# Performance work log

Measured on AMD Instinct MI355X. Metric: run time of the kernel, lower is better.

Reference implementation:

```python
import jax, jax.numpy as jnp
import numpy as np

B, T, E = 2, 2048, 2048
H, KV, D = 16, 4, 128
N_REP = H // KV
WINDOW = 512
BASE_THETA = 10000.0
MIN_VAL = -1e9


def _rope_cos_sin(seq_len, dim, dtype):
    inv_freq = 1.0 / (BASE_THETA ** (jnp.arange(0, dim, 2, dtype=jnp.float32) / dim))
    ang = jnp.arange(seq_len, dtype=jnp.float32)[:, None] * inv_freq[None, :]  # [T, D/2]
    return jnp.cos(ang).astype(dtype), jnp.sin(ang).astype(dtype)


def _apply_rope(x, cos, sin):
    # x: [B, T, h, D]; rotate-half convention
    x1, x2 = jnp.split(x, 2, axis=-1)
    c = cos[None, :, None, :]
    s = sin[None, :, None, :]
    return jnp.concatenate([x1 * c - x2 * s, x2 * c + x1 * s], axis=-1)


def setup_inputs() -> dict:
    key = jax.random.key(0)
    k1, k2, k3, k4, k5 = jax.random.split(key, 5)
    std = 0.02 / np.sqrt(2 * 24)
    return {
        "x": jax.random.normal(k1, (B, T, E), dtype=jnp.float32),
        "Wq": jax.random.normal(k2, (H * D, E), dtype=jnp.float32) * std,
        "Wk": jax.random.normal(k3, (KV * D, E), dtype=jnp.float32) * std,
        "Wv": jax.random.normal(k4, (KV * D, E), dtype=jnp.float32) * std,
        "Wo": jax.random.normal(k5, (E, E), dtype=jnp.float32) * std,
    }


def reference(x, Wq, Wk, Wv, Wo):
    b, t, e = x.shape
    scale = 1.0 / jnp.sqrt(jnp.float32(D))

    q = (x @ Wq.T).reshape(b, t, H, D)
    k = (x @ Wk.T).reshape(b, t, KV, D)
    v = (x @ Wv.T).reshape(b, t, KV, D)

    cos, sin = _rope_cos_sin(t, D, x.dtype)
    q = _apply_rope(q, cos, sin)
    k = _apply_rope(k, cos, sin)

    # GQA: repeat kv heads to match query heads
    k = jnp.repeat(k, N_REP, axis=2)  # [B, T, H, D]
    v = jnp.repeat(v, N_REP, axis=2)

    scores = jnp.einsum("bqhd,bkhd->bhqk", q, k) * scale  # [B, H, T, T]

    # sliding-window causal additive mask (offset=0)
    rows = jnp.arange(t)[:, None]
    cols = jnp.arange(t)[None, :]
    valid = (cols <= rows) & ((rows - cols) < WINDOW)
    mask = jnp.where(valid, 0.0, MIN_VAL).astype(x.dtype)  # [T, T]
    scores = scores + mask[None, None, :, :]

    attn = jax.nn.softmax(scores, axis=-1)
    out = jnp.einsum("bhqk,bkhd->bqhd", attn, v).reshape(b, t, H * D)
    return out @ Wo.T
```

## Files before the change

kernel.cpp:

```cpp
#include <hip/hip_runtime.h>
#include <hip/hip_bf16.h>
#include <cstdint>

#define TSEQ 2048
#define NB   2
#define NH   16
#define NKV  4
#define HD   128
#define EMB  2048
#define WIN  512

typedef unsigned short u16;
typedef __attribute__((ext_vector_type(8))) short s16x8;
typedef __attribute__((ext_vector_type(4))) float f32x4;
typedef __attribute__((ext_vector_type(16))) float f32x16;
typedef __attribute__((ext_vector_type(4))) unsigned short u16x4;
typedef __attribute__((ext_vector_type(8))) unsigned short u16x8;

__device__ __forceinline__ u16 f2bf(float x) {
    unsigned u = __builtin_bit_cast(unsigned, x);
    u += 0x7fffu + ((u >> 16) & 1u);
    return (u16)(u >> 16);
}
__device__ __forceinline__ float bf2f(u16 u) {
    return __builtin_bit_cast(float, ((unsigned)u) << 16);
}
__device__ __forceinline__ float ex2(float x) {
    return __builtin_amdgcn_exp2f(x);
}

__device__ __forceinline__ void gld_lds16(const void* g, void* l) {
    __builtin_amdgcn_global_load_lds(
        (__attribute__((address_space(1))) void*)(void*)(g),
        (__attribute__((address_space(3))) void*)(l),
        16, 0, 0);
}

__device__ __forceinline__ f32x4 mfma16(s16x8 a, s16x8 b, f32x4 c) {
    return __builtin_amdgcn_mfma_f32_16x16x32_bf16(a, b, c, 0, 0, 0);
}
__device__ __forceinline__ f32x16 mfma32(s16x8 a, s16x8 b, f32x16 c) {
    return __builtin_amdgcn_mfma_f32_32x32x16_bf16(a, b, c, 0, 0, 0);
}

template <int CTRL>
__device__ __forceinline__ float dpp_movf(float x) {
    return __builtin_bit_cast(float,
        __builtin_amdgcn_update_dpp(0, __builtin_bit_cast(int, x), CTRL, 0xF, 0xF, true));
}
__device__ __forceinline__ float dpp_max16(float x) {
    x = fmaxf(x, dpp_movf<0xB1>(x));
    x = fmaxf(x, dpp_movf<0x4E>(x));
    x = fmaxf(x, dpp_movf<0x128>(x));
    x = fmaxf(x, dpp_movf<0x124>(x));
    return x;
}
__device__ __forceinline__ float dpp_sum16(float x) {
    x += dpp_movf<0xB1>(x);
    x += dpp_movf<0x4E>(x);
    x += dpp_movf<0x128>(x);
    x += dpp_movf<0x124>(x);
    return x;
}

__global__ void cast_all(const float* __restrict__ x,  const float* __restrict__ wq,
                         const float* __restrict__ wk, const float* __restrict__ wv,
                         const float* __restrict__ wo,
                         u16* __restrict__ xb, u16* __restrict__ wqb,
                         u16* __restrict__ wkvb, u16* __restrict__ wob,
                         float* __restrict__ tab) {
    if (blockIdx.x >= 18432) {
        int i = (blockIdx.x - 18432) * 256 + threadIdx.x;
        int t = i >> 6, d = i & 63;
        float inv = __expf(-(float)d * (9.210340371976184f / 64.0f));
        float s, c;
        sincosf((float)t * inv, &s, &c);
        tab[i] = c;
        tab[131072 + i] = s;
        return;
    }
    long i = ((long)blockIdx.x * 256 + threadIdx.x) * 4;
    const float* s; u16* d; long off;
    if (i < 8388608L)        { s = x;  d = xb;             off = i; }
    else if (i < 12582912L)  { s = wq; d = wqb;            off = i - 8388608L; }
    else if (i < 13631488L)  { s = wk; d = wkvb;           off = i - 12582912L; }
    else if (i < 14680064L)  { s = wv; d = wkvb + 1048576; off = i - 13631488L; }
    else                     { s = wo; d = wob;            off = i - 14680064L; }
    float4 v = *(const float4*)(s + off);
    u16x4 o;
    o[0] = f2bf(v.x); o[1] = f2bf(v.y); o[2] = f2bf(v.z); o[3] = f2bf(v.w);
    *(u16x4*)(d + off) = o;
}

template <int MODE>
__global__ __launch_bounds__(256) void gemm_bt(const u16* __restrict__ A, const u16* __restrict__ B,
                                               void* __restrict__ Cp, u16* __restrict__ vtp,
                                               u16* __restrict__ kp,
                                               int M, int N, int K) {
    __shared__ __align__(16) u16 smem[16384];
    u16* As = smem;
    u16* Bs = smem + 8192;
    const int tid  = threadIdx.x;
    const int lane = tid & 63;
    const int w    = tid >> 6;
    const int l31  = lane & 31;
    const int half = lane >> 5;
    const int wr   = w >> 1, wc = w & 1;

    const int srow   = w * 8 + (lane >> 3);
    const int schunk = lane & 7;
    const u16* agp[4];
    const u16* bgp[4];
#pragma unroll
    for (int s = 0; s < 4; s++) {
        const int row = s * 32 + srow;
        const int sig = ((row >> 1) ^ (row >> 2)) & 7;
        agp[s] = A + (size_t)(blockIdx.y * 128 + row) * K + (schunk ^ sig) * 8;
        bgp[s] = B + (size_t)(blockIdx.x * 128 + row) * K + (schunk ^ sig) * 8;
    }

    int sigA[2], sigB[2];
#pragma unroll
    for (int i = 0; i < 2; i++) {
        const int ra = wr * 64 + i * 32 + l31;
        sigA[i] = ((ra >> 1) ^ (ra >> 2)) & 7;
        const int rb = wc * 64 + i * 32 + l31;
        sigB[i] = ((rb >> 1) ^ (rb >> 2)) & 7;
    }

    f32x16 acc[2][2];
#pragma unroll
    for (int i = 0; i < 2; i++)
#pragma unroll
        for (int j = 0; j < 2; j++)
#pragma unroll
            for (int r = 0; r < 16; r++)
                acc[i][j][r] = 0.f;

    for (int k0 = 0; k0 < K; k0 += 64) {
#pragma unroll
        for (int s = 0; s < 4; s++) {
            gld_lds16(agp[s], (char*)As + (s * 32 + w * 8) * 128);
            agp[s] += 64;
        }
#pragma unroll
        for (int s = 0; s < 4; s++) {
            gld_lds16(bgp[s], (char*)Bs + (s * 32 + w * 8) * 128);
            bgp[s] += 64;
        }
        __syncthreads();
        s16x8 af[2][4], bf[2][4];
#pragma unroll
        for (int i = 0; i < 2; i++)
#pragma unroll
            for (int ks = 0; ks < 4; ks++)
                af[i][ks] = *(const s16x8*)((char*)As + (wr * 64 + i * 32 + l31) * 128 +
                                            ((half + ks * 2) ^ sigA[i]) * 16);
#pragma unroll
        for (int j = 0; j < 2; j++)
#pragma unroll
            for (int ks = 0; ks < 4; ks++)
                bf[j][ks] = *(const s16x8*)((char*)Bs + (wc * 64 + j * 32 + l31) * 128 +
                                            ((half + ks * 2) ^ sigB[j]) * 16);
#pragma unroll
        for (int ks = 0; ks < 4; ks++)
#pragma unroll
            for (int i = 0; i < 2; i++)
#pragma unroll
                for (int j = 0; j < 2; j++)
                    acc[i][j] = mfma32(af[i][ks], bf[j][ks], acc[i][j]);
        __syncthreads();
    }

    const int row0 = blockIdx.y * 128 + wr * 64;
    const int col0 = blockIdx.x * 128 + wc * 64 + l31;

    if (MODE == 0) {
#pragma unroll
        for (int i = 0; i < 2; i++)
#pragma unroll
            for (int j = 0; j < 2; j++)
#pragma unroll
                for (int r = 0; r < 16; r++) {
                    const int crow = row0 + i * 32 + (r & 3) + 8 * (r >> 2) + 4 * half;
                    ((float*)Cp)[(size_t)crow * N + col0 + j * 32] = acc[i][j][r];
                }
    } else {
        if (blockIdx.x < 16) {
#pragma unroll
            for (int i = 0; i < 2; i++)
#pragma unroll
                for (int j = 0; j < 2; j++)
#pragma unroll
                    for (int r = 0; r < 16; r++) {
                        const int crow = row0 + i * 32 + (r & 3) + 8 * (r >> 2) + 4 * half;
                        ((u16*)Cp)[(size_t)crow * 2048 + col0 + j * 32] = f2bf(acc[i][j][r]);
                    }
        } else if (blockIdx.x < 20) {
            const int kcol0 = col0 - 2048;
#pragma unroll
            for (int i = 0; i < 2; i++)
#pragma unroll
                for (int j = 0; j < 2; j++)
#pragma unroll
                    for (int r = 0; r < 16; r++) {
                        const int crow = row0 + i * 32 + (r & 3) + 8 * (r >> 2) + 4 * half;
                        kp[(size_t)crow * 512 + kcol0 + j * 32] = f2bf(acc[i][j][r]);
                    }
        } else {
            const int kvi = blockIdx.x - 20;
            const int bb  = (blockIdx.y * 128) >> 11;
            const int tl0 = (blockIdx.y * 128) & (TSEQ - 1);
            u16* tr = smem;
#pragma unroll
            for (int p = 0; p < 2; p++) {
                __syncthreads();
                if (wc == p) {
#pragma unroll
                    for (int i = 0; i < 2; i++)
#pragma unroll
                        for (int j = 0; j < 2; j++)
#pragma unroll
                            for (int r = 0; r < 16; r++) {
                                const int tl = wr * 64 + i * 32 + (r & 3) + 8 * (r >> 2) + 4 * half;
                                tr[(j * 32 + l31) * 136 + tl] = f2bf(acc[i][j][r]);
                            }
                }
                __syncthreads();
#pragma unroll
                for (int s = 0; s < 4; s++) {
                    int slot = s * 256 + tid;
                    int dr = slot >> 4;
                    int tc = slot & 15;
                    u16x8 val = *(const u16x8*)(tr + dr * 136 + tc * 8);
                    *(u16x8*)(vtp + ((size_t)((bb * NKV + kvi) * HD + p * 64 + dr)) * TSEQ +
                              tl0 + tc * 8) = val;
                }
            }
        }
    }
}

__global__ void rope_k(u16* __restrict__ buf, const float* __restrict__ tab) {
    int i = blockIdx.x * 256 + threadIdx.x;
    int d   = i & 63;
    int hh  = (i >> 6) & 3;
    int row = i >> 8;
    int t   = row & (TSEQ - 1);
    size_t base = (size_t)row * 512 + hh * HD + d;
    float x1 = bf2f(buf[base]);
    float x2 = bf2f(buf[base + 64]);
    float c = tab[t * 64 + d];
    float s = tab[131072 + t * 64 + d];
    buf[base]      = f2bf(x1 * c - x2 * s);
    buf[base + 64] = f2bf(x2 * c + x1 * s);
}

__global__ __launch_bounds__(256, 4) void attn_kernel(const u16* __restrict__ qb, const u16* __restrict__ kb,
                                                      const u16* __restrict__ vt, const float* __restrict__ tab,
                                                      u16* __restrict__ ao) {
    __shared__ __align__(16) char smem[40960];
    u16* ks = (u16*)smem;
    u16* vs = (u16*)(smem + 16384);
    u16* Pl = (u16*)(smem + 32768);

    const int tid  = threadIdx.x;
    const int w    = tid >> 6;
    const int lane = tid & 63;
    const int l15  = lane & 15;
    const int quad = lane >> 4;
    const int id   = blockIdx.x;
    const int kv   = id & 3;
    const int b    = (id >> 2) & 1;
    const int q0   = (id >> 3) * 16;
    const int h    = kv * 4 + w;
    u16* Pw = Pl + w * 1024;
    const float scale2 = 0.1275174089593282f;

    const u16* kbase = kb + (size_t)b * TSEQ * 512 + kv * HD;
    const u16* vbase = vt + (size_t)(b * NKV + kv) * HD * TSEQ;

    s16x8 aq[4];
    {
        const u16* qrow = qb + (size_t)(b * TSEQ + q0 + l15) * EMB + h * HD + quad * 8;
        const float* ct = tab + (size_t)(q0 + l15) * 64 + quad * 8;
        float qf[4][8], cs[2][8], sn[2][8];
        *(float4*)(&cs[0][0]) = *(const float4*)(ct);
        *(float4*)(&cs[0][4]) = *(const float4*)(ct + 4);
        *(float4*)(&cs[1][0]) = *(const float4*)(ct + 32);
        *(float4*)(&cs[1][4]) = *(const float4*)(ct + 36);
        *(float4*)(&sn[0][0]) = *(const float4*)(ct + 131072);
        *(float4*)(&sn[0][4]) = *(const float4*)(ct + 131076);
        *(float4*)(&sn[1][0]) = *(const float4*)(ct + 131104);
        *(float4*)(&sn[1][4]) = *(const float4*)(ct + 131108);
#pragma unroll
        for (int c = 0; c < 4; c++)
#pragma unroll
            for (int e = 0; e < 8; e++)
                qf[c][e] = bf2f(qrow[c * 32 + e]);
#pragma unroll
        for (int c = 0; c < 2; c++)
#pragma unroll
            for (int e = 0; e < 8; e++) {
                float x1 = qf[c][e], x2 = qf[c + 2][e];
                qf[c][e]     = x1 * cs[c][e] - x2 * sn[c][e];
                qf[c + 2][e] = x2 * cs[c][e] + x1 * sn[c][e];
            }
#pragma unroll
        for (int c = 0; c < 4; c++)
#pragma unroll
            for (int e = 0; e < 8; e++)
                aq[c][e] = (short)f2bf(qf[c][e]);
    }

    f32x4 o[8];
#pragma unroll
    for (int n = 0; n < 8; n++) o[n] = f32x4{0.f, 0.f, 0.f, 0.f};
    float mrow[4] = {-1e30f, -1e30f, -1e30f, -1e30f};
    float lrow[4] = {0.f, 0.f, 0.f, 0.f};

    int kb0 = q0 - (WIN - 1);
    if (kb0 < 0) kb0 = 0;
    kb0 &= ~63;

    for (int kbi = kb0; kbi <= q0 + 15; kbi += 64) {
#pragma unroll
        for (int s = 0; s < 4; s++) {
            int slot = s * 256 + tid;
            int i    = slot >> 4;
            int lc   = (slot & 15) ^ (i & 7);
            gld_lds16(kbase + (size_t)(kbi + i) * 512 + lc * 8, (char*)ks + slot * 16);
        }
#pragma unroll
        for (int s = 0; s < 4; s++) {
            int slot = s * 256 + tid;
            int d    = slot >> 3;
            int lc   = (slot & 7) ^ (d & 7);
            gld_lds16(vbase + (size_t)d * TSEQ + kbi + lc * 8, (char*)vs + slot * 16);
        }
        __syncthreads();

        f32x4 sv[4];
#pragma unroll
        for (int kt = 0; kt < 4; kt++) sv[kt] = f32x4{0.f, 0.f, 0.f, 0.f};
        __builtin_amdgcn_s_setprio(1);
#pragma unroll
        for (int c = 0; c < 4; c++) {
            s16x8 bk[4];
#pragma unroll
            for (int kt = 0; kt < 4; kt++) {
                int sc = (c * 4 + quad) ^ (l15 & 7);
                bk[kt] = *(const s16x8*)(ks + (kt * 16 + l15) * 128 + sc * 8);
            }
#pragma unroll
            for (int kt = 0; kt < 4; kt++)
                sv[kt] = mfma16(aq[c], bk[kt], sv[kt]);
        }
        __builtin_amdgcn_s_setprio(0);

        const bool full = (kbi >= q0 - 496) && (kbi + 63 <= q0);
        float alpha[4], p[4][4];
#pragma unroll
        for (int r = 0; r < 4; r++) {
            const int row = q0 + quad * 4 + r;
            float v[4];
            if (full) {
#pragma unroll
                for (int kt = 0; kt < 4; kt++) v[kt] = sv[kt][r] * scale2;
            } else {
#pragma unroll
                for (int kt = 0; kt < 4; kt++) {
                    int cidx = kbi + kt * 16 + l15;
                    v[kt] = (cidx <= row && row - cidx < WIN) ? sv[kt][r] * scale2 : -1e30f;
                }
            }
            float mx = fmaxf(fmaxf(v[0], v[1]), fmaxf(v[2], v[3]));
            mx = dpp_max16(mx);
            float mnew = fmaxf(mrow[r], mx);
            alpha[r] = ex2(mrow[r] - mnew);
            float e0 = ex2(v[0] - mnew);
            float e1 = ex2(v[1] - mnew);
            float e2 = ex2(v[2] - mnew);
            float e3 = ex2(v[3] - mnew);
            float rs = (e0 + e1) + (e2 + e3);
            rs = dpp_sum16(rs);
            lrow[r] = lrow[r] * alpha[r] + rs;
            mrow[r] = mnew;
            p[0][r] = e0; p[1][r] = e1; p[2][r] = e2; p[3][r] = e3;
        }
#pragma unroll
        for (int n = 0; n < 8; n++) {
            o[n][0] *= alpha[0]; o[n][1] *= alpha[1];
            o[n][2] *= alpha[2]; o[n][3] *= alpha[3];
        }

#pragma unroll
        for (int r = 0; r < 4; r++)
#pragma unroll
            for (int kt = 0; kt < 4; kt++)
                Pw[(kt >> 1) * 512 + (quad * 4 + r) * 32 + (kt & 1) * 16 + l15] = f2bf(p[kt][r]);
        asm volatile("s_waitcnt lgkmcnt(0)" ::: "memory");
        s16x8 ap0 = *(const s16x8*)(Pw + l15 * 32 + quad * 8);
        s16x8 ap1 = *(const s16x8*)(Pw + 512 + l15 * 32 + quad * 8);

        __builtin_amdgcn_s_setprio(1);
#pragma unroll
        for (int n = 0; n < 8; n++) {
            int sc = quad ^ (l15 & 7);
            s16x8 bv = *(const s16x8*)(vs + (n * 16 + l15) * 64 + sc * 8);
            o[n] = mfma16(ap0, bv, o[n]);
        }
#pragma unroll
        for (int n = 0; n < 8; n++) {
            int sc = (4 + quad) ^ (l15 & 7);
            s16x8 bv = *(const s16x8*)(vs + (n * 16 + l15) * 64 + sc * 8);
            o[n] = mfma16(ap1, bv, o[n]);
        }
        __builtin_amdgcn_s_setprio(0);
        __syncthreads();
    }

    float linv[4];
#pragma unroll
    for (int r = 0; r < 4; r++) linv[r] = 1.0f / lrow[r];
    u16* Ow = (u16*)(smem + w * 4352);
#pragma unroll
    for (int n = 0; n < 8; n++)
#pragma unroll
        for (int r = 0; r < 4; r++)
            Ow[(quad * 4 + r) * 136 + n * 16 + l15] = f2bf(o[n][r] * linv[r]);
    asm volatile("s_waitcnt lgkmcnt(0)" ::: "memory");
#pragma unroll
    for (int s = 0; s < 4; s++) {
        int row = s * 4 + quad;
        u16x8 val = *(const u16x8*)(Ow + row * 136 + l15 * 8);
        *(u16x8*)(ao + (size_t)(b * TSEQ + q0 + row) * EMB + h * HD + l15 * 8) = val;
    }
}

extern "C" void kernel_launch(void* const* d_in, const int* in_sizes, int n_in,
                              void* d_out, int out_size, void* d_ws, size_t ws_size,
                              hipStream_t stream) {
    const float* x  = (const float*)d_in[0];
    const float* Wq = (const float*)d_in[1];
    const float* Wk = (const float*)d_in[2];
    const float* Wv = (const float*)d_in[3];
    const float* Wo = (const float*)d_in[4];
    float* out = (float*)d_out;

    u16* ws   = (u16*)d_ws;
    u16* xb   = ws;
    u16* wqb  = ws + 8388608L;
    u16* wkvb = ws + 12582912L;
    u16* wob  = ws + 14680064L;
    u16* qb   = ws + 18874368L;
    u16* kbuf = ws + 27262976L;
    u16* vt   = ws + 29360128L;
    float* tab = (float*)(ws + 31457280L);
    u16* ao   = xb;

    cast_all<<<18944, 256, 0, stream>>>(x, Wq, Wk, Wv, Wo, xb, wqb, wkvb, wob, tab);

    gemm_bt<3><<<dim3(24, 32), 256, 0, stream>>>(xb, wqb, qb, vt, kbuf, 4096, 3072, 2048);

    rope_k<<<4096, 256, 0, stream>>>(kbuf, tab);

    attn_kernel<<<1024, 256, 0, stream>>>(qb, kbuf, vt, tab, ao);

    gemm_bt<0><<<dim3(16, 32), 256, 0, stream>>>(ao, wob, out, nullptr, nullptr, 4096, 2048, 2048);
}
```

Before: 261.3 us.

## Prefetch next K/V tile into registers during attention compute

Replaces the direct global-to-LDS loads of each K/V tile with a register-staged software pipeline. The next tile is loaded into registers at the start of each iteration, overlapping with the QK and PV MFMA work, and written to LDS after the trailing barrier. Address computation is hoisted out of the loop. This adds register pressure from eight 16-byte vectors and gives up the async LDS-direct load path.

```diff
diff --git a/kernel.cpp b/kernel.cpp
--- a/kernel.cpp
+++ b/kernel.cpp
@@ -322,23 +322,49 @@
     int kb0 = q0 - (WIN - 1);
     if (kb0 < 0) kb0 = 0;
     kb0 &= ~63;
-
-    for (int kbi = kb0; kbi <= q0 + 15; kbi += 64) {
-#pragma unroll
-        for (int s = 0; s < 4; s++) {
-            int slot = s * 256 + tid;
-            int i    = slot >> 4;
-            int lc   = (slot & 15) ^ (i & 7);
-            gld_lds16(kbase + (size_t)(kbi + i) * 512 + lc * 8, (char*)ks + slot * 16);
-        }
-#pragma unroll
-        for (int s = 0; s < 4; s++) {
-            int slot = s * 256 + tid;
-            int d    = slot >> 3;
-            int lc   = (slot & 7) ^ (d & 7);
-            gld_lds16(vbase + (size_t)d * TSEQ + kbi + lc * 8, (char*)vs + slot * 16);
-        }
+    const int kend = q0 + 15;
+
+    const int sl0 = tid, sl1 = 256 + tid, sl2 = 512 + tid, sl3 = 768 + tid;
+    const u16* kp0 = kbase + (size_t)(sl0 >> 4) * 512 + (size_t)(((sl0 & 15) ^ ((sl0 >> 4) & 7)) * 8);
+    const u16* kp1 = kbase + (size_t)(sl1 >> 4) * 512 + (size_t)(((sl1 & 15) ^ ((sl1 >> 4) & 7)) * 8);
+    const u16* kp2 = kbase + (size_t)(sl2 >> 4) * 512 + (size_t)(((sl2 & 15) ^ ((sl2 >> 4) & 7)) * 8);
+    const u16* kp3 = kbase + (size_t)(sl3 >> 4) * 512 + (size_t)(((sl3 & 15) ^ ((sl3 >> 4) & 7)) * 8);
+    const u16* vp0 = vbase + (size_t)(sl0 >> 3) * TSEQ + (size_t)(((sl0 & 7) ^ ((sl0 >> 3) & 7)) * 8);
+    const u16* vp1 = vbase + (size_t)(sl1 >> 3) * TSEQ + (size_t)(((sl1 & 7) ^ ((sl1 >> 3) & 7)) * 8);
+    const u16* vp2 = vbase + (size_t)(sl2 >> 3) * TSEQ + (size_t)(((sl2 & 7) ^ ((sl2 >> 3) & 7)) * 8);
+    const u16* vp3 = vbase + (size_t)(sl3 >> 3) * TSEQ + (size_t)(((sl3 & 7) ^ ((sl3 >> 3) & 7)) * 8);
+    u16* kd0 = (u16*)((char*)ks + sl0 * 16);
+    u16* kd1 = (u16*)((char*)ks + sl1 * 16);
+    u16* kd2 = (u16*)((char*)ks + sl2 * 16);
+    u16* kd3 = (u16*)((char*)ks + sl3 * 16);
+    u16* vd0 = (u16*)((char*)vs + sl0 * 16);
+    u16* vd1 = (u16*)((char*)vs + sl1 * 16);
+    u16* vd2 = (u16*)((char*)vs + sl2 * 16);
+    u16* vd3 = (u16*)((char*)vs + sl3 * 16);
+
+    u16x8 kr0, kr1, kr2, kr3, vr0, vr1, vr2, vr3;
+    {
+        const size_t ko = (size_t)kb0 * 512;
+        kr0 = *(const u16x8*)(kp0 + ko); kr1 = *(const u16x8*)(kp1 + ko);
+        kr2 = *(const u16x8*)(kp2 + ko); kr3 = *(const u16x8*)(kp3 + ko);
+        vr0 = *(const u16x8*)(vp0 + kb0); vr1 = *(const u16x8*)(vp1 + kb0);
+        vr2 = *(const u16x8*)(vp2 + kb0); vr3 = *(const u16x8*)(vp3 + kb0);
+        *(u16x8*)kd0 = kr0; *(u16x8*)kd1 = kr1; *(u16x8*)kd2 = kr2; *(u16x8*)kd3 = kr3;
+        *(u16x8*)vd0 = vr0; *(u16x8*)vd1 = vr1; *(u16x8*)vd2 = vr2; *(u16x8*)vd3 = vr3;
+    }
+
+    for (int kbi = kb0; kbi <= kend; kbi += 64) {
         __syncthreads();
+        const bool have_next = (kbi + 64 <= kend);
+        if (have_next) {
+            const size_t ko = (size_t)(kbi + 64) * 512;
+            const int    vo = kbi + 64;
+            kr0 = *(const u16x8*)(kp0 + ko); kr1 = *(const u16x8*)(kp1 + ko);
+            kr2 = *(const u16x8*)(kp2 + ko); kr3 = *(const u16x8*)(kp3 + ko);
+            vr0 = *(const u16x8*)(vp0 + vo); vr1 = *(const u16x8*)(vp1 + vo);
+            vr2 = *(const u16x8*)(vp2 + vo); vr3 = *(const u16x8*)(vp3 + vo);
+            __builtin_amdgcn_sched_barrier(0);
+        }
 
         f32x4 sv[4];
 #pragma unroll
@@ -417,7 +443,12 @@
             o[n] = mfma16(ap1, bv, o[n]);
         }
         __builtin_amdgcn_s_setprio(0);
+
         __syncthreads();
+        if (have_next) {
+            *(u16x8*)kd0 = kr0; *(u16x8*)kd1 = kr1; *(u16x8*)kd2 = kr2; *(u16x8*)kd3 = kr3;
+            *(u16x8*)vd0 = vr0; *(u16x8*)vd1 = vr1; *(u16x8*)vd2 = vr2; *(u16x8*)vd3 = vr3;
+        }
     }
 
     float linv[4];
```

After: 304.1 us. +16.4%, slower.
